# Kernel optimization log

Measured on AMD Instinct MI355X. Metric: run time of the kernel, lower is better.

Reference implementation:

```python
import jax, jax.numpy as jnp
import numpy as np

CUTOFF = 5.0
N_RBF = 20

A = 50000
F = 128
E = 500000


def setup_inputs() -> dict:
    key = jax.random.key(0)
    ks = jax.random.split(key, 10)
    return {
        "vectors": jax.random.normal(ks[0], (A, 3, F), dtype=jnp.float32),
        "scalars": jax.random.normal(ks[1], (A, 1, F), dtype=jnp.float32),
        "directions": jax.random.normal(ks[2], (E, 3), dtype=jnp.float32),
        "idx_i": jax.random.randint(ks[3], (E,), 0, A),
        "idx_j": jax.random.randint(ks[4], (E,), 0, A),
        "W1": jax.random.normal(ks[5], (F, F), dtype=jnp.float32) / np.sqrt(F),
        "b1": jnp.zeros((F,), dtype=jnp.float32),
        "W2": jax.random.normal(ks[6], (F, 3 * F), dtype=jnp.float32) / np.sqrt(F),
        "b2": jnp.zeros((3 * F,), dtype=jnp.float32),
        "Wr": jax.random.normal(ks[7], (N_RBF, 3 * F), dtype=jnp.float32) / np.sqrt(N_RBF),
        "br": jnp.zeros((3 * F,), dtype=jnp.float32),
    }


def reference(vectors, scalars, directions, idx_i, idx_j, W1, b1, W2, b2, Wr, br):
    feat = scalars.shape[-1]
    n_nodes = vectors.shape[0]
    n_rbf = Wr.shape[0]

    s = jax.nn.silu(scalars @ W1 + b1) @ W2 + b2

    # edge norms: E x 1
    norm_r = jnp.sqrt(jnp.sum(directions * directions, axis=-1, keepdims=True))

    # radial basis: sin(k*pi/rc * |r|)/|r|  -> E x n
    rr = jnp.arange(1, n_rbf + 1, dtype=directions.dtype)
    rbf = jnp.sin(rr * (jnp.pi / CUTOFF) * norm_r) / norm_r
    r = rbf @ Wr + br  # E x 3F

    # cosine cutoff with hard mask (min(delta,0)/delta == 1 inside cutoff, 0 outside)
    delta = norm_r - CUTOFF
    mask = jnp.minimum(delta, 0.0) / delta
    fc = 0.5 * (jnp.cos(jnp.pi * norm_r / CUTOFF) + 1.0) * mask
    r = fc * r  # E x 3F

    combined = s[idx_i] * r[:, None, :]
    delta_s, delta_v1, delta_v2 = jnp.split(combined, 3, axis=-1)

    delta_v = vectors[idx_i] * delta_v1 + delta_v2 * (directions / norm_r)[:, :, None]

    # scatter-add back to nodes
    delta_s = jax.ops.segment_sum(delta_s, idx_j, num_segments=n_nodes)
    delta_v = jax.ops.segment_sum(delta_v, idx_j, num_segments=n_nodes)
    return delta_v, delta_s
```

## Files before the change

### kernel.cpp

```cpp
#include <hip/hip_runtime.h>
#include <math.h>

#define A_NODES 50000
#define FEAT 128
#define EDGES 500000
#define NRBF 20
#define CUTOFF_F 5.0f
#define PI_OVER_CUTOFF 0.6283185307179586f

typedef unsigned int uint32;
typedef unsigned short ushort16;

__device__ __forceinline__ ushort16 f2bf(float f) {
    union { float f; uint32 u; } v; v.f = f;
    uint32 r = (v.u + 0x7fffu + ((v.u >> 16) & 1u)) >> 16;
    return (ushort16)r;
}
__device__ __forceinline__ uint32 packbf(float a, float b) {
    return (uint32)f2bf(a) | ((uint32)f2bf(b) << 16);
}
__device__ __forceinline__ float bf_lo(uint32 u) { return __uint_as_float(u << 16); }
__device__ __forceinline__ float bf_hi(uint32 u) { return __uint_as_float(u & 0xffff0000u); }

#if __has_builtin(__builtin_amdgcn_fdot2_f32_bf16)
typedef __bf16 bf16x2 __attribute__((ext_vector_type(2)));
__device__ __forceinline__ float dot2(uint32 a, uint32 b, float c) {
    return __builtin_amdgcn_fdot2_f32_bf16(
        __builtin_bit_cast(bf16x2, a), __builtin_bit_cast(bf16x2, b), c, false);
}
#else
__device__ __forceinline__ float dot2(uint32 a, uint32 b, float c) {
    return fmaf(bf_hi(a), bf_hi(b), fmaf(bf_lo(a), bf_lo(b), c));
}
#endif

__global__ __launch_bounds__(128) void node_mlp_kernel(
    const float* __restrict__ scalars,
    const float* __restrict__ W1, const float* __restrict__ b1,
    const float* __restrict__ W2, const float* __restrict__ b2,
    ushort16* __restrict__ s_bf)
{
    __shared__ float sc[8][128];
    __shared__ float hid[8][128];
    const int tx = threadIdx.x;
    const int base = blockIdx.x * 8;

    #pragma unroll
    for (int n = 0; n < 8; ++n)
        sc[n][tx] = scalars[(size_t)(base + n) * FEAT + tx];
    __syncthreads();

    float h[8];
    {
        const float bb = b1[tx];
        #pragma unroll
        for (int n = 0; n < 8; ++n) h[n] = bb;
    }
    #pragma unroll 4
    for (int k = 0; k < 128; ++k) {
        const float w = W1[k * 128 + tx];
        #pragma unroll
        for (int n = 0; n < 8; ++n) h[n] = fmaf(sc[n][k], w, h[n]);
    }
    #pragma unroll
    for (int n = 0; n < 8; ++n) {
        const float x = h[n];
        hid[n][tx] = x / (1.0f + __expf(-x));
    }
    __syncthreads();

    float a0[8], a1[8], a2[8];
    {
        const float bb0 = b2[tx], bb1 = b2[tx + 128], bb2 = b2[tx + 256];
        #pragma unroll
        for (int n = 0; n < 8; ++n) { a0[n] = bb0; a1[n] = bb1; a2[n] = bb2; }
    }
    #pragma unroll 2
    for (int k = 0; k < 128; ++k) {
        const float w0 = W2[k * 384 + tx];
        const float w1 = W2[k * 384 + tx + 128];
        const float w2 = W2[k * 384 + tx + 256];
        #pragma unroll
        for (int n = 0; n < 8; ++n) {
            const float hh = hid[n][k];
            a0[n] = fmaf(hh, w0, a0[n]);
            a1[n] = fmaf(hh, w1, a1[n]);
            a2[n] = fmaf(hh, w2, a2[n]);
        }
    }
    #pragma unroll
    for (int n = 0; n < 8; ++n) {
        ushort16* row = s_bf + (size_t)(base + n) * 384;
        row[tx]       = f2bf(a0[n]);
        row[tx + 128] = f2bf(a1[n]);
        row[tx + 256] = f2bf(a2[n]);
    }
}

__global__ __launch_bounds__(256) void vec_cvt_kernel(
    const float* __restrict__ vin, uint32* __restrict__ vbf)
{
    const int t = blockIdx.x * 256 + threadIdx.x;
    const size_t n2 = (size_t)A_NODES * 384 / 2;
    if (t < (int)n2) {
        const float a = vin[2 * (size_t)t];
        const float b = vin[2 * (size_t)t + 1];
        vbf[t] = packbf(a, b);
    }
}

__global__ __launch_bounds__(256) void wr_pack_kernel(
    const float* __restrict__ Wr, uint32* __restrict__ wrpk)
{
    const int t = blockIdx.x * 256 + threadIdx.x;
    if (t < 10 * 384) {
        const int m = t / 384, col = t % 384;
        wrpk[t] = packbf(Wr[(2 * m) * 384 + col], Wr[(2 * m + 1) * 384 + col]);
    }
}

__global__ __launch_bounds__(256) void hist_kernel(
    const int* __restrict__ idx_j, int* __restrict__ hist)
{
    const int e = blockIdx.x * 256 + threadIdx.x;
    if (e < EDGES) atomicAdd(&hist[idx_j[e]], 1);
}

__global__ __launch_bounds__(1024) void scan_kernel(
    const int* __restrict__ hist, int* __restrict__ offsets,
    int* __restrict__ cursor)
{
    __shared__ int part[1024];
    const int t = threadIdx.x;
    const int CH = (A_NODES + 1023) / 1024;

    int sum = 0;
    for (int k = 0; k < CH; ++k) {
        const int idx = t * CH + k;
        if (idx < A_NODES) sum += hist[idx];
    }
    part[t] = sum;
    __syncthreads();
    for (int off = 1; off < 1024; off <<= 1) {
        const int v = (t >= off) ? part[t - off] : 0;
        __syncthreads();
        part[t] += v;
        __syncthreads();
    }
    int run = part[t] - sum;
    for (int k = 0; k < CH; ++k) {
        const int idx = t * CH + k;
        if (idx < A_NODES) {
            offsets[idx] = run;
            cursor[idx]  = run;
            run += hist[idx];
        }
    }
    if (t == 0) offsets[A_NODES] = EDGES;
}

__global__ __launch_bounds__(256) void scatter_kernel(
    const int* __restrict__ idx_j, int* __restrict__ cursor,
    int* __restrict__ order)
{
    const int e = blockIdx.x * 256 + threadIdx.x;
    if (e < EDGES) {
        const int pos = atomicAdd(&cursor[idx_j[e]], 1);
        order[pos] = e;
    }
}

__global__ __launch_bounds__(256) void edge_prep_kernel(
    const float* __restrict__ directions,
    const int* __restrict__ idx_i, const int* __restrict__ order,
    float* __restrict__ edata)
{
    const int p = blockIdx.x * 256 + threadIdx.x;
    if (p >= EDGES) return;
    const int e = order[p];
    const int i = idx_i[e];
    const float d0 = directions[(size_t)e * 3 + 0];
    const float d1 = directions[(size_t)e * 3 + 1];
    const float d2 = directions[(size_t)e * 3 + 2];
    const float nr   = sqrtf(d0 * d0 + d1 * d1 + d2 * d2);
    const float invn = 1.0f / nr;
    const float x = PI_OVER_CUTOFF * nr;
    float sx, cx;
    sincosf(x, &sx, &cx);
    const float fc = (nr < CUTOFF_F) ? 0.5f * (cx + 1.0f) : 0.0f;
    const float scale = invn * fc;
    const float twoc = 2.0f * cx;

    float out16[16];
    float s_odd = sx;
    float s_prev = 0.0f;
    #pragma unroll
    for (int m = 0; m < 10; ++m) {
        const float s_even = twoc * s_odd - s_prev;
        out16[m] = __uint_as_float(packbf(s_odd * scale, s_even * scale));
        const float s_next = twoc * s_even - s_odd;
        s_prev = s_even;
        s_odd  = s_next;
    }
    out16[10] = d0 * invn;
    out16[11] = d1 * invn;
    out16[12] = d2 * invn;
    out16[13] = fc;
    out16[14] = __int_as_float(i);
    out16[15] = 0.0f;

    float4* dst = (float4*)(edata + (size_t)p * 16);
    dst[0] = make_float4(out16[0],  out16[1],  out16[2],  out16[3]);
    dst[1] = make_float4(out16[4],  out16[5],  out16[6],  out16[7]);
    dst[2] = make_float4(out16[8],  out16[9],  out16[10], out16[11]);
    dst[3] = make_float4(out16[12], out16[13], out16[14], out16[15]);
}

template <int VBF>
__global__ __launch_bounds__(256) void gather_kernel(
    const ushort16* __restrict__ s_bf,
    const ushort16* __restrict__ v_bf,
    const float* __restrict__ vectors_f32,
    const uint32* __restrict__ wrpk, const float* __restrict__ br,
    const float* __restrict__ edata,
    const int* __restrict__ offsets,
    float* __restrict__ out_v, float* __restrict__ out_s)
{
    const int lane   = threadIdx.x & 63;
    const int wv     = __builtin_amdgcn_readfirstlane(threadIdx.x >> 6);
    const int nsub   = wv >> 1;
    const int parity = wv & 1;
    const int j      = blockIdx.x * 2 + nsub;
    const int c0     = lane * 2;

    uint32 wA[30], wB[30];
    #pragma unroll
    for (int s = 0; s < 3; ++s)
        #pragma unroll
        for (int m = 0; m < 10; ++m) {
            wA[s * 10 + m] = wrpk[m * 384 + s * 128 + c0];
            wB[s * 10 + m] = wrpk[m * 384 + s * 128 + c0 + 1];
        }
    const float brA0 = br[c0],       brB0 = br[c0 + 1];
    const float brA1 = br[128 + c0], brB1 = br[129 + c0];
    const float brA2 = br[256 + c0], brB2 = br[257 + c0];

    const int beg = offsets[j];
    const int end = offsets[j + 1];

    float accsA = 0.f, accsB = 0.f;
    float avA0 = 0.f, avA1 = 0.f, avA2 = 0.f;
    float avB0 = 0.f, avB1 = 0.f, avB2 = 0.f;

    for (int p = beg + parity; p < end; p += 2) {
        const float* ed = edata + (size_t)p * 16;
        uint32 rb[10];
        #pragma unroll
        for (int m = 0; m < 10; ++m) rb[m] = __float_as_uint(ed[m]);
        const float u0 = ed[10], u1 = ed[11], u2 = ed[12], fcv = ed[13];
        const int   i  = __float_as_int(ed[14]);

        const ushort16* srow = s_bf + (size_t)i * 384;
        const uint32 s0 = *(const uint32*)(srow + c0);
        const uint32 s1 = *(const uint32*)(srow + 128 + c0);
        const uint32 s2 = *(const uint32*)(srow + 256 + c0);

        float rA0 = fcv * brA0, rA1 = fcv * brA1, rA2 = fcv * brA2;
        float rB0 = fcv * brB0, rB1 = fcv * brB1, rB2 = fcv * brB2;
        #pragma unroll
        for (int m = 0; m < 10; ++m) {
            const uint32 rm = rb[m];
            rA0 = dot2(rm, wA[m],      rA0);
            rA1 = dot2(rm, wA[10 + m], rA1);
            rA2 = dot2(rm, wA[20 + m], rA2);
            rB0 = dot2(rm, wB[m],      rB0);
            rB1 = dot2(rm, wB[10 + m], rB1);
            rB2 = dot2(rm, wB[20 + m], rB2);
        }

        const float sA0 = bf_lo(s0), sB0 = bf_hi(s0);
        const float sA1 = bf_lo(s1), sB1 = bf_hi(s1);
        const float sA2 = bf_lo(s2), sB2 = bf_hi(s2);

        accsA = fmaf(sA0, rA0, accsA);
        accsB = fmaf(sB0, rB0, accsB);
        const float gA1 = sA1 * rA1, gA2 = sA2 * rA2;
        const float gB1 = sB1 * rB1, gB2 = sB2 * rB2;

        float vA0, vB0, vA1, vB1, vA2, vB2;
        if (VBF) {
            const ushort16* vrow = v_bf + (size_t)i * 384;
            const uint32 v0 = *(const uint32*)(vrow + c0);
            const uint32 v1 = *(const uint32*)(vrow + 128 + c0);
            const uint32 v2 = *(const uint32*)(vrow + 256 + c0);
            vA0 = bf_lo(v0); vB0 = bf_hi(v0);
            vA1 = bf_lo(v1); vB1 = bf_hi(v1);
            vA2 = bf_lo(v2); vB2 = bf_hi(v2);
        } else {
            const float* vrow = vectors_f32 + (size_t)i * 384;
            vA0 = vrow[c0];       vB0 = vrow[c0 + 1];
            vA1 = vrow[128 + c0]; vB1 = vrow[129 + c0];
            vA2 = vrow[256 + c0]; vB2 = vrow[257 + c0];
        }

        avA0 = fmaf(vA0, gA1, fmaf(gA2, u0, avA0));
        avB0 = fmaf(vB0, gB1, fmaf(gB2, u0, avB0));
        avA1 = fmaf(vA1, gA1, fmaf(gA2, u1, avA1));
        avB1 = fmaf(vB1, gB1, fmaf(gB2, u1, avB1));
        avA2 = fmaf(vA2, gA1, fmaf(gA2, u2, avA2));
        avB2 = fmaf(vB2, gB1, fmaf(gB2, u2, avB2));
    }

    __shared__ float red[4][64][9];
    float* slot = red[wv][lane];
    slot[0] = accsA; slot[1] = accsB;
    slot[2] = avA0;  slot[3] = avB0;
    slot[4] = avA1;  slot[5] = avB1;
    slot[6] = avA2;  slot[7] = avB2;
    __syncthreads();

    if (parity == 0) {
        const float* o = red[wv | 1][lane];
        float2* os = (float2*)(out_s + (size_t)j * 128 + c0);
        *os = make_float2(accsA + o[0], accsB + o[1]);
        float* ov = out_v + (size_t)j * 384;
        *(float2*)(ov + c0)       = make_float2(avA0 + o[2], avB0 + o[3]);
        *(float2*)(ov + 128 + c0) = make_float2(avA1 + o[4], avB1 + o[5]);
        *(float2*)(ov + 256 + c0) = make_float2(avA2 + o[6], avB2 + o[7]);
    }
}

extern "C" void kernel_launch(void* const* d_in, const int* in_sizes, int n_in,
                              void* d_out, int out_size, void* d_ws, size_t ws_size,
                              hipStream_t stream) {
    const float* vectors    = (const float*)d_in[0];
    const float* scalars    = (const float*)d_in[1];
    const float* directions = (const float*)d_in[2];
    const int*   idx_i      = (const int*)d_in[3];
    const int*   idx_j      = (const int*)d_in[4];
    const float* W1         = (const float*)d_in[5];
    const float* b1         = (const float*)d_in[6];
    const float* W2         = (const float*)d_in[7];
    const float* b2         = (const float*)d_in[8];
    const float* Wr         = (const float*)d_in[9];
    const float* br         = (const float*)d_in[10];

    float* out_v = (float*)d_out;
    float* out_s = out_v + (size_t)A_NODES * 3 * FEAT;

    char* ws = (char*)d_ws;
    ushort16* s_bf = (ushort16*)ws;  ws += (size_t)A_NODES * 384 * 2;
    float* edata   = (float*)ws;     ws += (size_t)EDGES * 16 * 4;
    uint32* wrpk   = (uint32*)ws;    ws += (size_t)10 * 384 * 4;
    int* hist      = (int*)ws;       ws += (size_t)A_NODES * 4;
    int* offsets   = (int*)ws;       ws += (((size_t)(A_NODES + 1) * 4 + 15) & ~(size_t)15);
    int* cursor    = (int*)ws;       ws += (size_t)A_NODES * 4;
    int* order     = (int*)ws;       ws += (size_t)EDGES * 4;
    ushort16* v_bf = (ushort16*)ws;  ws += (size_t)A_NODES * 384 * 2;

    const int use_vbf = ((size_t)(ws - (char*)d_ws) <= ws_size) ? 1 : 0;

    hipMemsetAsync(hist, 0, (size_t)A_NODES * 4, stream);

    node_mlp_kernel<<<A_NODES / 8, 128, 0, stream>>>(scalars, W1, b1, W2, b2, s_bf);
    if (use_vbf)
        vec_cvt_kernel<<<(A_NODES * 384 / 2 + 255) / 256, 256, 0, stream>>>(vectors, (uint32*)v_bf);
    wr_pack_kernel<<<15, 256, 0, stream>>>(Wr, wrpk);

    hist_kernel<<<(EDGES + 255) / 256, 256, 0, stream>>>(idx_j, hist);
    scan_kernel<<<1, 1024, 0, stream>>>(hist, offsets, cursor);
    scatter_kernel<<<(EDGES + 255) / 256, 256, 0, stream>>>(idx_j, cursor, order);
    edge_prep_kernel<<<(EDGES + 255) / 256, 256, 0, stream>>>(directions, idx_i, order, edata);

    if (use_vbf)
        gather_kernel<1><<<A_NODES / 2, 256, 0, stream>>>(
            s_bf, v_bf, vectors, wrpk, br, edata, offsets, out_v, out_s);
    else
        gather_kernel<0><<<A_NODES / 2, 256, 0, stream>>>(
            s_bf, v_bf, vectors, wrpk, br, edata, offsets, out_v, out_s);
}
```

Baseline: 647.7 us.

## Use MFMA for node MLP, fuse scatter into edge prep, one node per block

The node MLP now runs on bf16 MFMA instructions with weights pre-packed into a fragment layout by a combined pack kernel, instead of a scalar FMA loop. The separate scatter kernel is folded into edge_prep, which claims its sorted slot with an atomic and writes edata there directly, so the order array and one pass are gone. The gather kernel now gives each block one destination node with four waves striding over its edges, prefetches the next edge record, loads the weights only when the node has edges, and uses nontemporal output stores. The trade-offs are bf16 rounding of the MLP inputs and hidden activations, and more blocks with less work each in the gather kernel.

```diff
diff --git a/kernel.cpp b/kernel.cpp
--- a/kernel.cpp
+++ b/kernel.cpp
@@ -10,6 +10,9 @@
 
 typedef unsigned int uint32;
 typedef unsigned short ushort16;
+typedef short bf16x8 __attribute__((ext_vector_type(8)));
+typedef float f32x4 __attribute__((ext_vector_type(4)));
+typedef float f32x2 __attribute__((ext_vector_type(2)));
 
 __device__ __forceinline__ ushort16 f2bf(float f) {
     union { float f; uint32 u; } v; v.f = f;
@@ -34,66 +37,110 @@
 }
 #endif
 
-__global__ __launch_bounds__(128) void node_mlp_kernel(
+__global__ __launch_bounds__(256) void pack_kernel(
+    const float* __restrict__ W1, const float* __restrict__ W2,
+    const float* __restrict__ Wr,
+    ushort16* __restrict__ w1pk, ushort16* __restrict__ w2pk,
+    uint32* __restrict__ wrpk)
+{
+    const int t = blockIdx.x * 256 + threadIdx.x;
+    if (t < 16384) {
+        const int jj = t & 7, l = (t >> 3) & 63, kk = (t >> 9) & 3, nt = t >> 11;
+        const int col = (l & 15) + 16 * nt;
+        const int k   = kk * 32 + (l >> 4) * 8 + jj;
+        w1pk[t] = f2bf(W1[k * 128 + col]);
+    } else if (t < 16384 + 49152) {
+        const int u = t - 16384;
+        const int jj = u & 7, l = (u >> 3) & 63, kk = (u >> 9) & 3, nt = u >> 11;
+        const int col = (l & 15) + 16 * nt;
+        const int k   = kk * 32 + (l >> 4) * 8 + jj;
+        w2pk[u] = f2bf(W2[k * 384 + col]);
+    } else if (t < 16384 + 49152 + 3840) {
+        const int u = t - 16384 - 49152;
+        const int m = u / 384, col = u % 384;
+        wrpk[u] = packbf(Wr[(2 * m) * 384 + col], Wr[(2 * m + 1) * 384 + col]);
+    }
+}
+
+__global__ __launch_bounds__(256) void node_mlp_kernel(
     const float* __restrict__ scalars,
-    const float* __restrict__ W1, const float* __restrict__ b1,
-    const float* __restrict__ W2, const float* __restrict__ b2,
+    const ushort16* __restrict__ w1pk, const float* __restrict__ bias1,
+    const ushort16* __restrict__ w2pk, const float* __restrict__ bias2,
     ushort16* __restrict__ s_bf)
 {
-    __shared__ float sc[8][128];
-    __shared__ float hid[8][128];
-    const int tx = threadIdx.x;
-    const int base = blockIdx.x * 8;
-
+    __shared__ ushort16 sc[16][136];
+    __shared__ ushort16 hd[16][136];
+    const int tx   = threadIdx.x;
+    const int lane = tx & 63;
+    const int wv   = tx >> 6;
+    const int base = blockIdx.x * 16;
+
+    {
+        const int row = tx >> 4;
+        const int cs  = (tx & 15) * 8;
+        const float* src = scalars + (size_t)(base + row) * FEAT + cs;
+        const float4 f0 = *(const float4*)src;
+        const float4 f1 = *(const float4*)(src + 4);
+        bf16x8 tmp;
+        tmp[0] = (short)f2bf(f0.x); tmp[1] = (short)f2bf(f0.y);
+        tmp[2] = (short)f2bf(f0.z); tmp[3] = (short)f2bf(f0.w);
+        tmp[4] = (short)f2bf(f1.x); tmp[5] = (short)f2bf(f1.y);
+        tmp[6] = (short)f2bf(f1.z); tmp[7] = (short)f2bf(f1.w);
+        *(bf16x8*)&sc[row][cs] = tmp;
+    }
+    __syncthreads();
+
+    const int arow = lane & 15;
+    const int kgrp = lane >> 4;
+
+    f32x4 acc0 = {0.f, 0.f, 0.f, 0.f};
+    f32x4 acc1 = {0.f, 0.f, 0.f, 0.f};
     #pragma unroll
-    for (int n = 0; n < 8; ++n)
-        sc[n][tx] = scalars[(size_t)(base + n) * FEAT + tx];
+    for (int kk = 0; kk < 4; ++kk) {
+        const bf16x8 a  = *(const bf16x8*)&sc[arow][kk * 32 + kgrp * 8];
+        const bf16x8 b0 = *(const bf16x8*)(w1pk + (((size_t)(wv * 2 + 0) * 4 + kk) * 64 + lane) * 8);
+        const bf16x8 b1 = *(const bf16x8*)(w1pk + (((size_t)(wv * 2 + 1) * 4 + kk) * 64 + lane) * 8);
+        acc0 = __builtin_amdgcn_mfma_f32_16x16x32_bf16(a, b0, acc0, 0, 0, 0);
+        acc1 = __builtin_amdgcn_mfma_f32_16x16x32_bf16(a, b1, acc1, 0, 0, 0);
+    }
+    {
+        const int c0 = wv * 32 + (lane & 15);
+        const int c1 = c0 + 16;
+        const float bb0 = bias1[c0], bb1 = bias1[c1];
+        #pragma unroll
+        for (int r = 0; r < 4; ++r) {
+            const int row = kgrp * 4 + r;
+            float x0 = acc0[r] + bb0;
+            float x1 = acc1[r] + bb1;
+            x0 = x0 / (1.0f + __expf(-x0));
+            x1 = x1 / (1.0f + __expf(-x1));
+            hd[row][c0] = f2bf(x0);
+            hd[row][c1] = f2bf(x1);
+        }
+    }
     __syncthreads();
 
-    float h[8];
-    {
-        const float bb = b1[tx];
+    f32x4 acc[6];
+    #pragma unroll
+    for (int n = 0; n < 6; ++n) acc[n] = (f32x4){0.f, 0.f, 0.f, 0.f};
+    #pragma unroll
+    for (int kk = 0; kk < 4; ++kk) {
+        const bf16x8 a = *(const bf16x8*)&hd[arow][kk * 32 + kgrp * 8];
         #pragma unroll
-        for (int n = 0; n < 8; ++n) h[n] = bb;
-    }
-    #pragma unroll 4
-    for (int k = 0; k < 128; ++k) {
-        const float w = W1[k * 128 + tx];
+        for (int n = 0; n < 6; ++n) {
+            const bf16x8 b = *(const bf16x8*)(w2pk + (((size_t)(wv * 6 + n) * 4 + kk) * 64 + lane) * 8);
+            acc[n] = __builtin_amdgcn_mfma_f32_16x16x32_bf16(a, b, acc[n], 0, 0, 0);
+        }
+    }
+    #pragma unroll
+    for (int n = 0; n < 6; ++n) {
+        const int col = (wv * 6 + n) * 16 + (lane & 15);
+        const float bb = bias2[col];
         #pragma unroll
-        for (int n = 0; n < 8; ++n) h[n] = fmaf(sc[n][k], w, h[n]);
-    }
-    #pragma unroll
-    for (int n = 0; n < 8; ++n) {
-        const float x = h[n];
-        hid[n][tx] = x / (1.0f + __expf(-x));
-    }
-    __syncthreads();
-
-    float a0[8], a1[8], a2[8];
-    {
-        const float bb0 = b2[tx], bb1 = b2[tx + 128], bb2 = b2[tx + 256];
-        #pragma unroll
-        for (int n = 0; n < 8; ++n) { a0[n] = bb0; a1[n] = bb1; a2[n] = bb2; }
-    }
-    #pragma unroll 2
-    for (int k = 0; k < 128; ++k) {
-        const float w0 = W2[k * 384 + tx];
-        const float w1 = W2[k * 384 + tx + 128];
-        const float w2 = W2[k * 384 + tx + 256];
-        #pragma unroll
-        for (int n = 0; n < 8; ++n) {
-            const float hh = hid[n][k];
-            a0[n] = fmaf(hh, w0, a0[n]);
-            a1[n] = fmaf(hh, w1, a1[n]);
-            a2[n] = fmaf(hh, w2, a2[n]);
-        }
-    }
-    #pragma unroll
-    for (int n = 0; n < 8; ++n) {
-        ushort16* row = s_bf + (size_t)(base + n) * 384;
-        row[tx]       = f2bf(a0[n]);
-        row[tx + 128] = f2bf(a1[n]);
-        row[tx + 256] = f2bf(a2[n]);
+        for (int r = 0; r < 4; ++r) {
+            const int row = kgrp * 4 + r;
+            s_bf[(size_t)(base + row) * 384 + col] = f2bf(acc[n][r] + bb);
+        }
     }
 }
 
@@ -106,16 +153,6 @@
         const float a = vin[2 * (size_t)t];
         const float b = vin[2 * (size_t)t + 1];
         vbf[t] = packbf(a, b);
-    }
-}
-
-__global__ __launch_bounds__(256) void wr_pack_kernel(
-    const float* __restrict__ Wr, uint32* __restrict__ wrpk)
-{
-    const int t = blockIdx.x * 256 + threadIdx.x;
-    if (t < 10 * 384) {
-        const int m = t / 384, col = t % 384;
-        wrpk[t] = packbf(Wr[(2 * m) * 384 + col], Wr[(2 * m + 1) * 384 + col]);
     }
 }
 
@@ -159,26 +196,17 @@
     if (t == 0) offsets[A_NODES] = EDGES;
 }
 
-__global__ __launch_bounds__(256) void scatter_kernel(
-    const int* __restrict__ idx_j, int* __restrict__ cursor,
-    int* __restrict__ order)
-{
-    const int e = blockIdx.x * 256 + threadIdx.x;
-    if (e < EDGES) {
-        const int pos = atomicAdd(&cursor[idx_j[e]], 1);
-        order[pos] = e;
-    }
-}
-
 __global__ __launch_bounds__(256) void edge_prep_kernel(
     const float* __restrict__ directions,
-    const int* __restrict__ idx_i, const int* __restrict__ order,
+    const int* __restrict__ idx_i, const int* __restrict__ idx_j,
+    int* __restrict__ cursor,
     float* __restrict__ edata)
 {
-    const int p = blockIdx.x * 256 + threadIdx.x;
-    if (p >= EDGES) return;
-    const int e = order[p];
-    const int i = idx_i[e];
+    const int e = blockIdx.x * 256 + threadIdx.x;
+    if (e >= EDGES) return;
+    const int j   = idx_j[e];
+    const int pos = atomicAdd(&cursor[j], 1);
+    const int i   = idx_i[e];
     const float d0 = directions[(size_t)e * 3 + 0];
     const float d1 = directions[(size_t)e * 3 + 1];
     const float d2 = directions[(size_t)e * 3 + 2];
@@ -209,7 +237,7 @@
     out16[14] = __int_as_float(i);
     out16[15] = 0.0f;
 
-    float4* dst = (float4*)(edata + (size_t)p * 16);
+    float4* dst = (float4*)(edata + (size_t)pos * 16);
     dst[0] = make_float4(out16[0],  out16[1],  out16[2],  out16[3]);
     dst[1] = make_float4(out16[4],  out16[5],  out16[6],  out16[7]);
     dst[2] = make_float4(out16[8],  out16[9],  out16[10], out16[11]);
@@ -217,7 +245,7 @@
 }
 
 template <int VBF>
-__global__ __launch_bounds__(256) void gather_kernel(
+__global__ __launch_bounds__(256, 4) void gather_kernel(
     const ushort16* __restrict__ s_bf,
     const ushort16* __restrict__ v_bf,
     const float* __restrict__ vectors_f32,
@@ -226,24 +254,10 @@
     const int* __restrict__ offsets,
     float* __restrict__ out_v, float* __restrict__ out_s)
 {
-    const int lane   = threadIdx.x & 63;
-    const int wv     = __builtin_amdgcn_readfirstlane(threadIdx.x >> 6);
-    const int nsub   = wv >> 1;
-    const int parity = wv & 1;
-    const int j      = blockIdx.x * 2 + nsub;
-    const int c0     = lane * 2;
-
-    uint32 wA[30], wB[30];
-    #pragma unroll
-    for (int s = 0; s < 3; ++s)
-        #pragma unroll
-        for (int m = 0; m < 10; ++m) {
-            wA[s * 10 + m] = wrpk[m * 384 + s * 128 + c0];
-            wB[s * 10 + m] = wrpk[m * 384 + s * 128 + c0 + 1];
-        }
-    const float brA0 = br[c0],       brB0 = br[c0 + 1];
-    const float brA1 = br[128 + c0], brB1 = br[129 + c0];
-    const float brA2 = br[256 + c0], brB2 = br[257 + c0];
+    const int lane = threadIdx.x & 63;
+    const int wv   = __builtin_amdgcn_readfirstlane(threadIdx.x >> 6);
+    const int j    = blockIdx.x;
+    const int c0   = lane * 2;
 
     const int beg = offsets[j];
     const int end = offsets[j + 1];
@@ -252,40 +266,36 @@
     float avA0 = 0.f, avA1 = 0.f, avA2 = 0.f;
     float avB0 = 0.f, avB1 = 0.f, avB2 = 0.f;
 
-    for (int p = beg + parity; p < end; p += 2) {
-        const float* ed = edata + (size_t)p * 16;
-        uint32 rb[10];
+    uint32 wA[30], wB[30];
+    float brA0 = 0.f, brB0 = 0.f, brA1 = 0.f, brB1 = 0.f, brA2 = 0.f, brB2 = 0.f;
+
+    int p = beg + wv;
+    float4 cA, cB, cC, cD;
+
+    if (p < end) {
         #pragma unroll
-        for (int m = 0; m < 10; ++m) rb[m] = __float_as_uint(ed[m]);
-        const float u0 = ed[10], u1 = ed[11], u2 = ed[12], fcv = ed[13];
-        const int   i  = __float_as_int(ed[14]);
+        for (int s = 0; s < 3; ++s)
+            #pragma unroll
+            for (int m = 0; m < 10; ++m) {
+                wA[s * 10 + m] = wrpk[m * 384 + s * 128 + c0];
+                wB[s * 10 + m] = wrpk[m * 384 + s * 128 + c0 + 1];
+            }
+        brA0 = br[c0];       brB0 = br[c0 + 1];
+        brA1 = br[128 + c0]; brB1 = br[129 + c0];
+        brA2 = br[256 + c0]; brB2 = br[257 + c0];
+
+        const float4* s0p = (const float4*)(edata + (size_t)p * 16);
+        cA = s0p[0]; cB = s0p[1]; cC = s0p[2]; cD = s0p[3];
+    }
+
+    while (p < end) {
+        const int pn = p + 4;
+        const int i  = __float_as_int(cD.z);
 
         const ushort16* srow = s_bf + (size_t)i * 384;
         const uint32 s0 = *(const uint32*)(srow + c0);
         const uint32 s1 = *(const uint32*)(srow + 128 + c0);
         const uint32 s2 = *(const uint32*)(srow + 256 + c0);
-
-        float rA0 = fcv * brA0, rA1 = fcv * brA1, rA2 = fcv * brA2;
-        float rB0 = fcv * brB0, rB1 = fcv * brB1, rB2 = fcv * brB2;
-        #pragma unroll
-        for (int m = 0; m < 10; ++m) {
-            const uint32 rm = rb[m];
-            rA0 = dot2(rm, wA[m],      rA0);
-            rA1 = dot2(rm, wA[10 + m], rA1);
-            rA2 = dot2(rm, wA[20 + m], rA2);
-            rB0 = dot2(rm, wB[m],      rB0);
-            rB1 = dot2(rm, wB[10 + m], rB1);
-            rB2 = dot2(rm, wB[20 + m], rB2);
-        }
-
-        const float sA0 = bf_lo(s0), sB0 = bf_hi(s0);
-        const float sA1 = bf_lo(s1), sB1 = bf_hi(s1);
-        const float sA2 = bf_lo(s2), sB2 = bf_hi(s2);
-
-        accsA = fmaf(sA0, rA0, accsA);
-        accsB = fmaf(sB0, rB0, accsB);
-        const float gA1 = sA1 * rA1, gA2 = sA2 * rA2;
-        const float gB1 = sB1 * rB1, gB2 = sB2 * rB2;
 
         float vA0, vB0, vA1, vB1, vA2, vB2;
         if (VBF) {
@@ -303,12 +313,51 @@
             vA2 = vrow[256 + c0]; vB2 = vrow[257 + c0];
         }
 
+        const size_t pf = (size_t)(pn < end ? pn : p) * 16;
+        const float4* sn = (const float4*)(edata + pf);
+        const float4 nA = sn[0], nB = sn[1], nC = sn[2], nD = sn[3];
+
+        const float u0 = cC.z, u1 = cC.w, u2 = cD.x;
+        const float fcv = cD.y;
+
+        uint32 rb[10] = {
+            __float_as_uint(cA.x), __float_as_uint(cA.y),
+            __float_as_uint(cA.z), __float_as_uint(cA.w),
+            __float_as_uint(cB.x), __float_as_uint(cB.y),
+            __float_as_uint(cB.z), __float_as_uint(cB.w),
+            __float_as_uint(cC.x), __float_as_uint(cC.y) };
+
+        float rA0 = fcv * brA0, rA1 = fcv * brA1, rA2 = fcv * brA2;
+        float rB0 = fcv * brB0, rB1 = fcv * brB1, rB2 = fcv * brB2;
+        #pragma unroll
+        for (int m = 0; m < 10; ++m) {
+            const uint32 rm = rb[m];
+            rA0 = dot2(rm, wA[m],      rA0);
+            rA1 = dot2(rm, wA[10 + m], rA1);
+            rA2 = dot2(rm, wA[20 + m], rA2);
+            rB0 = dot2(rm, wB[m],      rB0);
+            rB1 = dot2(rm, wB[10 + m], rB1);
+            rB2 = dot2(rm, wB[20 + m], rB2);
+        }
+
+        const float sA0 = bf_lo(s0), sB0 = bf_hi(s0);
+        const float sA1 = bf_lo(s1), sB1 = bf_hi(s1);
+        const float sA2 = bf_lo(s2), sB2 = bf_hi(s2);
+
+        accsA = fmaf(sA0, rA0, accsA);
+        accsB = fmaf(sB0, rB0, accsB);
+        const float gA1 = sA1 * rA1, gA2 = sA2 * rA2;
+        const float gB1 = sB1 * rB1, gB2 = sB2 * rB2;
+
         avA0 = fmaf(vA0, gA1, fmaf(gA2, u0, avA0));
         avB0 = fmaf(vB0, gB1, fmaf(gB2, u0, avB0));
         avA1 = fmaf(vA1, gA1, fmaf(gA2, u1, avA1));
         avB1 = fmaf(vB1, gB1, fmaf(gB2, u1, avB1));
         avA2 = fmaf(vA2, gA1, fmaf(gA2, u2, avA2));
         avB2 = fmaf(vB2, gB1, fmaf(gB2, u2, avB2));
+
+        cA = nA; cB = nB; cC = nC; cD = nD;
+        p = pn;
     }
 
     __shared__ float red[4][64][9];
@@ -319,14 +368,24 @@
     slot[6] = avA2;  slot[7] = avB2;
     __syncthreads();
 
-    if (parity == 0) {
-        const float* o = red[wv | 1][lane];
-        float2* os = (float2*)(out_s + (size_t)j * 128 + c0);
-        *os = make_float2(accsA + o[0], accsB + o[1]);
+    if (wv == 0) {
+        const float* o1 = red[1][lane];
+        const float* o2 = red[2][lane];
+        const float* o3 = red[3][lane];
+        f32x2 t;
+        t.x = accsA + o1[0] + o2[0] + o3[0];
+        t.y = accsB + o1[1] + o2[1] + o3[1];
+        __builtin_nontemporal_store(t, (f32x2*)(out_s + (size_t)j * 128 + c0));
         float* ov = out_v + (size_t)j * 384;
-        *(float2*)(ov + c0)       = make_float2(avA0 + o[2], avB0 + o[3]);
-        *(float2*)(ov + 128 + c0) = make_float2(avA1 + o[4], avB1 + o[5]);
-        *(float2*)(ov + 256 + c0) = make_float2(avA2 + o[6], avB2 + o[7]);
+        t.x = avA0 + o1[2] + o2[2] + o3[2];
+        t.y = avB0 + o1[3] + o2[3] + o3[3];
+        __builtin_nontemporal_store(t, (f32x2*)(ov + c0));
+        t.x = avA1 + o1[4] + o2[4] + o3[4];
+        t.y = avB1 + o1[5] + o2[5] + o3[5];
+        __builtin_nontemporal_store(t, (f32x2*)(ov + 128 + c0));
+        t.x = avA2 + o1[6] + o2[6] + o3[6];
+        t.y = avB2 + o1[7] + o2[7] + o3[7];
+        __builtin_nontemporal_store(t, (f32x2*)(ov + 256 + c0));
     }
 }
 
@@ -352,30 +411,31 @@
     ushort16* s_bf = (ushort16*)ws;  ws += (size_t)A_NODES * 384 * 2;
     float* edata   = (float*)ws;     ws += (size_t)EDGES * 16 * 4;
     uint32* wrpk   = (uint32*)ws;    ws += (size_t)10 * 384 * 4;
+    ushort16* w1pk = (ushort16*)ws;  ws += (size_t)16384 * 2;
+    ushort16* w2pk = (ushort16*)ws;  ws += (size_t)49152 * 2;
     int* hist      = (int*)ws;       ws += (size_t)A_NODES * 4;
     int* offsets   = (int*)ws;       ws += (((size_t)(A_NODES + 1) * 4 + 15) & ~(size_t)15);
     int* cursor    = (int*)ws;       ws += (size_t)A_NODES * 4;
-    int* order     = (int*)ws;       ws += (size_t)EDGES * 4;
     ushort16* v_bf = (ushort16*)ws;  ws += (size_t)A_NODES * 384 * 2;
 
     const int use_vbf = ((size_t)(ws - (char*)d_ws) <= ws_size) ? 1 : 0;
 
     hipMemsetAsync(hist, 0, (size_t)A_NODES * 4, stream);
 
-    node_mlp_kernel<<<A_NODES / 8, 128, 0, stream>>>(scalars, W1, b1, W2, b2, s_bf);
+    pack_kernel<<<271, 256, 0, stream>>>(W1, W2, Wr, w1pk, w2pk, wrpk);
+    node_mlp_kernel<<<A_NODES / 16, 256, 0, stream>>>(scalars, w1pk, b1, w2pk, b2, s_bf);
     if (use_vbf)
         vec_cvt_kernel<<<(A_NODES * 384 / 2 + 255) / 256, 256, 0, stream>>>(vectors, (uint32*)v_bf);
-    wr_pack_kernel<<<15, 256, 0, stream>>>(Wr, wrpk);
 
     hist_kernel<<<(EDGES + 255) / 256, 256, 0, stream>>>(idx_j, hist);
     scan_kernel<<<1, 1024, 0, stream>>>(hist, offsets, cursor);
-    scatter_kernel<<<(EDGES + 255) / 256, 256, 0, stream>>>(idx_j, cursor, order);
-    edge_prep_kernel<<<(EDGES + 255) / 256, 256, 0, stream>>>(directions, idx_i, order, edata);
+    edge_prep_kernel<<<(EDGES + 255) / 256, 256, 0, stream>>>(
+        directions, idx_i, idx_j, cursor, edata);
 
     if (use_vbf)
-        gather_kernel<1><<<A_NODES / 2, 256, 0, stream>>>(
+        gather_kernel<1><<<A_NODES, 256, 0, stream>>>(
             s_bf, v_bf, vectors, wrpk, br, edata, offsets, out_v, out_s);
     else
-        gather_kernel<0><<<A_NODES / 2, 256, 0, stream>>>(
+        gather_kernel<0><<<A_NODES, 256, 0, stream>>>(
             s_bf, v_bf, vectors, wrpk, br, edata, offsets, out_v, out_s);
 }
```

Measured after the change: 613.2 us. 1.06x faster.
